# Performance work log

Hardware: AMD Instinct MI355X
Metric: run time of the kernel (lower is better)

Reference implementation:

```python
import jax, jax.numpy as jnp
import numpy as np

T = 32            # num_tsteps
B = 8192          # batch_size
W_IN0, W_OUT0 = 36, 18
W_IN1, W_OUT1 = 18, 8
TILE0, TILE1 = 2, 1
BETA = (0.95, 0.95)
TH = (0.55, 0.25)
Q = 15000.0       # sephia mrr_Q
ER_DB = 20.0      # sephia extinction ratio
IL_DB = 0.0       # sephia insertion loss
SHIFT_PM = -250.0 # sephia resonance shift per unit spike
P_UNITY = 1e-4    # dbm_to_watt(-10): optical power per WDM channel at unit input


def _lif(inp, mem, beta, th):
    # snntorch Leaky, reset_mechanism='zero', reset_delay=True:
    # reset decided from incoming mem, membrane zeroed before leak+integrate.
    reset = (mem > th).astype(inp.dtype)
    mem_new = (beta * mem + inp) * (1.0 - reset)
    spk = (mem_new > th).astype(inp.dtype)
    return spk, mem_new


def _allpass(spk, wl_nm):
    # All-pass MRR modulator: spike shifts the ring resonance by SHIFT_PM.
    # Normalized detuning delta = shift / (FWHM/2), FWHM = lambda / Q.
    fwhm_pm = wl_nm * 1e3 / Q                      # [C]
    delta = (spk * SHIFT_PM) / (0.5 * fwhm_pm)     # [B, C]
    gamma = 10.0 ** (-ER_DB / 20.0)                # on-resonance amplitude (ER)
    il = 10.0 ** (-IL_DB / 20.0)                   # insertion loss factor
    return (il * (1j * delta + gamma) / (1j * delta + 1.0)).astype(jnp.complex64)


def setup_inputs() -> dict:
    key = jax.random.key(0)
    ks = jax.random.split(key, 6)
    return {
        "x_in": jax.random.uniform(ks[0], (T, B, W_IN0), jnp.float32),
        "W0": jax.random.uniform(ks[1], (TILE0, W_IN0 // TILE0, W_OUT0 * 2 // TILE0), jnp.float32),
        "d0": jax.random.normal(ks[2], (TILE0, W_OUT0 // TILE0), jnp.float32) * 5e3,
        "W1": jax.random.uniform(ks[3], (TILE1, W_IN1 // TILE1, W_OUT1 * 2 // TILE1), jnp.float32),
        "d1": jax.random.normal(ks[4], (TILE1, W_OUT1 // TILE1), jnp.float32) * 5e3,
        "peak_powers_dbm": jax.random.uniform(ks[5], (W_IN0,), jnp.float32, -15.0, -5.0),
    }


def reference(x_in, W0, d0, W1, d1, peak_powers_dbm):
    wl0 = 1550.0 + 0.8 * jnp.arange(W_OUT0, dtype=jnp.float32)   # MRR resonance wavelengths (nm)
    # sephia_inputs: sqrt(dbm_to_watt(P_dbm) * 1e6) field amplitude per channel
    amp0 = jnp.sqrt((10.0 ** (peak_powers_dbm[:W_OUT0] / 10.0) / 1000.0) * 1e6)
    S0 = W_OUT0 * 2 // TILE0   # 18 spatial channels after EO broadcast
    S1 = W_OUT1 * 2 // TILE1   # 16 spatial channels into layer 1

    def step(carry, x_t):
        mem0, mem1 = carry
        b = x_t.shape[0]
        # --- EO conversion + layer 0 MRR weight bank (power domain) ---
        p_in = x_t * P_UNITY                                     # [B, 36] optical power
        p0 = jnp.broadcast_to(p_in[:, :, None], (b, W_IN0, S0)).reshape(b, TILE0, W_IN0 // TILE0, S0)
        I0 = jnp.einsum('btws,tws->bts', p0, W0)                 # photocurrents [B,2,18]
        cur0 = ((I0[..., 0::2] - I0[..., 1::2]) * d0).reshape(b, W_OUT0)  # balanced PDs + Diagonal
        spk0, mem0 = _lif(cur0, mem0, BETA[0], TH[0])
        # --- SEPhIA all-pass MRR modulation of comb lines ---
        lo = _allpass(spk0, wl0) * amp0.astype(jnp.complex64)    # [B, 18] complex field
        pw0 = jnp.abs(lo) ** 2                                   # detected power == spike record
        # --- post-SEPhIA broadcast + layer 1 weight bank ---
        p1 = jnp.broadcast_to(pw0[:, :, None], (b, W_IN1, S1)).reshape(b, TILE1, W_IN1 // TILE1, S1)
        I1 = jnp.einsum('btws,tws->bts', p1, W1)                 # [B,1,16]
        cur1 = ((I1[..., 0::2] - I1[..., 1::2]) * d1).reshape(b, W_OUT1)
        spk1, mem1 = _lif(cur1, mem1, BETA[1], TH[1])
        return (mem0, mem1), (pw0, spk1, mem0, mem1)

    mem0 = jnp.zeros((x_in.shape[1], W_OUT0), x_in.dtype)
    mem1 = jnp.zeros((x_in.shape[1], W_OUT1), x_in.dtype)
    _, (spks0, spks1, mems0, mems1) = jax.lax.scan(step, (mem0, mem1), x_in)
    return spks0, spks1, mems0, mems1
```

## Files before the change

kernel.cpp:

```cpp
#include <hip/hip_runtime.h>


namespace {
constexpr int Tn = 32;
constexpr int Bn = 8192;
constexpr int O_PW = 0;
constexpr int O_S1 = Tn * Bn * 18;
constexpr int O_M0 = O_S1 + Tn * Bn * 8;
constexpr int O_M1 = O_M0 + Tn * Bn * 18;
}

__global__ __launch_bounds__(256, 1)
void oesnn_kernel(const float* __restrict__ x_in,
                  const float* __restrict__ W0g,
                  const float* __restrict__ d0g,
                  const float* __restrict__ W1g,
                  const float* __restrict__ d1g,
                  const float* __restrict__ peakg,
                  float* __restrict__ out)
{
    const int lt  = threadIdx.x & 63;
    const int tid = blockIdx.x * 256 + threadIdx.x;
    const int b   = tid >> 3;
    const int sub = tid & 7;
    const int tl  = sub >> 2;
    const int q   = sub & 3;
    const int j0  = (q == 0) ? 0 : (2 * q + 1);
    const int nj  = (q == 0) ? 3 : 2;

    float w0e[3][18], w0o[3][18], dd0[3], pon[3], poff[3];
    #pragma unroll
    for (int j = 0; j < 3; ++j) {
        const int jc = (j < nj) ? (j0 + j) : j0;
        dd0[j] = d0g[tl * 9 + jc];
        #pragma unroll
        for (int w = 0; w < 18; ++w) {
            const float2 p = *(const float2*)(W0g + ((tl * 18 + w) * 18 + 2 * jc));
            w0e[j][w] = p.x;
            w0o[j][w] = p.y;
        }
        const int c = tl * 9 + jc;
        const float wl    = 1550.0f + 0.8f * (float)c;
        const float halfw = 0.5f * (wl * 1e3f / 15000.0f);
        const float amp   = sqrtf((exp10f(peakg[c] / 10.0f) / 1000.0f) * 1e6f);
        {
            const float lr = 0.1f * amp;
            const float a  = sqrtf(lr * lr);
            poff[j] = a * a;
        }
        {
            const float delta = -250.0f / halfw;
            const float den = fmaf(delta, delta, 1.0f);
            const float qr  = fmaf(delta, delta, 0.1f) / den;
            const float qi  = (delta - 0.1f * delta) / den;
            const float lr = qr * amp, li = qi * amp;
            const float a  = sqrtf(fmaf(lr, lr, li * li));
            pon[j] = a * a;
        }
    }

    float w1e[18], w1o[18];
    #pragma unroll
    for (int w = 0; w < 18; ++w) {
        const float2 pp = *(const float2*)(W1g + w * 16 + 2 * sub);
        w1e[w] = pp.x;
        w1o[w] = pp.y;
    }
    const float dd1 = d1g[sub];

    const int basel = lt & ~7;

    float pon_f[18], poff_f[18];
    #pragma unroll
    for (int c = 0; c < 18; ++c) {
        const int tlc = c / 9, jc2 = c % 9;
        const int qo  = (jc2 < 3) ? 0 : ((jc2 - 1) / 2);
        const int st  = (qo == 0) ? 0 : (2 * qo + 1);
        const int r   = jc2 - st;
        pon_f[c]  = __shfl(pon[r],  basel + tlc * 4 + qo, 64);
        poff_f[c] = __shfl(poff[r], basel + tlc * 4 + qo, 64);
    }

    float dd1p = dd1;
    #pragma unroll
    for (int j = 0; j < 3; ++j) {
        #pragma unroll
        for (int w = 0; w < 18; ++w) {
            asm volatile("" : "+v"(w0e[j][w]));
            asm volatile("" : "+v"(w0o[j][w]));
        }
        asm volatile("" : "+v"(dd0[j]));
        asm volatile("" : "+v"(pon[j]));
        asm volatile("" : "+v"(poff[j]));
    }
    #pragma unroll
    for (int w = 0; w < 18; ++w) {
        asm volatile("" : "+v"(w1e[w]));
        asm volatile("" : "+v"(w1o[w]));
        asm volatile("" : "+v"(pon_f[w]));
        asm volatile("" : "+v"(poff_f[w]));
    }
    asm volatile("" : "+v"(dd1p));

    float mem0[3] = {0.f, 0.f, 0.f};
    float mem1 = 0.f;

    const float* xp = x_in + (size_t)b * 36 + tl * 18;
    float* opw = out + O_PW + (size_t)b * 18 + tl * 9 + j0;
    float* om0 = out + O_M0 + (size_t)b * 18 + tl * 9 + j0;
    float* os1 = out + O_S1 + (size_t)b * 8 + sub;
    float* om1 = out + O_M1 + (size_t)b * 8 + sub;

    float2 xv[9];
    #pragma unroll
    for (int k = 0; k < 9; ++k) xv[k] = *(const float2*)(xp + 2 * k);

    #pragma unroll 1
    for (int t = 0; t < Tn; ++t) {
        float p[18];
        #pragma unroll
        for (int k = 0; k < 9; ++k) {
            p[2 * k]     = xv[k].x * 1e-4f;
            p[2 * k + 1] = xv[k].y * 1e-4f;
        }
        xp += Bn * 36;
        if (t < Tn - 1) {
            #pragma unroll
            for (int k = 0; k < 9; ++k) xv[k] = *(const float2*)(xp + 2 * k);
        }

        float pwv[3];
        int   spk[3];
        #pragma unroll
        for (int j = 0; j < 3; ++j) {
            float se = 0.f, so = 0.f;
            #pragma unroll
            for (int w = 0; w < 18; ++w) {
                se = fmaf(p[w], w0e[j][w], se);
                so = fmaf(p[w], w0o[j][w], so);
            }
            const float c0 = (se - so) * dd0[j];
            const float m  = mem0[j];
            const float m2 = (m > 0.55f) ? 0.0f : fmaf(0.95f, m, c0);
            mem0[j] = m2;
            spk[j]  = (m2 > 0.55f) ? 1 : 0;
            pwv[j]  = spk[j] ? pon[j] : poff[j];
        }

        #pragma unroll
        for (int j = 0; j < 3; ++j) {
            if (j < nj) {
                opw[j] = pwv[j];
                om0[j] = mem0[j];
            }
        }

        unsigned long long bm0 = __ballot(spk[0]);
        unsigned long long bm1 = __ballot(spk[1]);
        unsigned long long bm2 = __ballot(spk[2]);
        const unsigned int g0 = (unsigned int)(bm0 >> basel);
        const unsigned int g1 = (unsigned int)(bm1 >> basel);
        const unsigned int g2 = (unsigned int)(bm2 >> basel);

        float i1e = 0.f, i1o = 0.f;
        #pragma unroll
        for (int c = 0; c < 18; ++c) {
            const int tlc = c / 9, jc2 = c % 9;
            const int qo  = (jc2 < 3) ? 0 : ((jc2 - 1) / 2);
            const int st  = (qo == 0) ? 0 : (2 * qo + 1);
            const int r   = jc2 - st;
            const unsigned int gm = (r == 0) ? g0 : ((r == 1) ? g1 : g2);
            const float pwc = ((gm >> (tlc * 4 + qo)) & 1u) ? pon_f[c] : poff_f[c];
            i1e = fmaf(pwc, w1e[c], i1e);
            i1o = fmaf(pwc, w1o[c], i1o);
        }

        const float c1 = (i1e - i1o) * dd1p;
        const float m  = mem1;
        const float m2 = (m > 0.25f) ? 0.0f : fmaf(0.95f, m, c1);
        mem1 = m2;
        *os1 = (m2 > 0.25f) ? 1.0f : 0.0f;
        *om1 = m2;

        opw += Bn * 18;
        om0 += Bn * 18;
        os1 += Bn * 8;
        om1 += Bn * 8;
    }
}

extern "C" void kernel_launch(void* const* d_in, const int* in_sizes, int n_in,
                              void* d_out, int out_size, void* d_ws, size_t ws_size,
                              hipStream_t stream) {
    (void)in_sizes; (void)n_in; (void)out_size; (void)d_ws; (void)ws_size;
    const float* x  = (const float*)d_in[0];
    const float* W0 = (const float*)d_in[1];
    const float* d0 = (const float*)d_in[2];
    const float* W1 = (const float*)d_in[3];
    const float* d1 = (const float*)d_in[4];
    const float* pk = (const float*)d_in[5];
    float* out = (float*)d_out;

    dim3 grid(Bn * 8 / 256), block(256);
    hipLaunchKernelGGL(oesnn_kernel, grid, block, 0, stream,
                       x, W0, d0, W1, d1, pk, out);
}
```

Baseline: 120.5 us.

## Stage x_in loads and pw/mem0 stores through per-wave LDS for coalescing

Each wavefront now stages four timesteps of its 8-batch x_in slab into a double-buffered LDS region with coalesced float4 loads. Per-thread inputs are read from LDS instead of strided global float2 loads. The pw0 and mem0 outputs are buffered in LDS and written back as contiguous float4 rows every four steps. This targets uncoalesced global traffic, at the cost of more LDS use, intra-wave LDS ordering without explicit barriers, and bursty store phases.

```diff
diff --git a/kernel.cpp b/kernel.cpp
--- a/kernel.cpp
+++ b/kernel.cpp
@@ -8,6 +8,9 @@
 constexpr int O_S1 = Tn * Bn * 18;
 constexpr int O_M0 = O_S1 + Tn * Bn * 8;
 constexpr int O_M1 = O_M0 + Tn * Bn * 18;
+constexpr int WSLAB = 3456;
+constexpr int PWOFF = 2304;
+constexpr int M0OFF = 2880;
 }
 
 __global__ __launch_bounds__(256, 1)
@@ -27,6 +30,11 @@
     const int q   = sub & 3;
     const int j0  = (q == 0) ? 0 : (2 * q + 1);
     const int nj  = (q == 0) ? 3 : 2;
+    const int e   = lt >> 3;
+    const int b0  = (tid & ~63) >> 3;
+
+    __shared__ float lds[4 * WSLAB];
+    float* wl = lds + (threadIdx.x >> 6) * WSLAB;
 
     float w0e[3][18], w0o[3][18], dd0[3], pon[3], poff[3];
     #pragma unroll
@@ -40,8 +48,8 @@
             w0o[j][w] = p.y;
         }
         const int c = tl * 9 + jc;
-        const float wl    = 1550.0f + 0.8f * (float)c;
-        const float halfw = 0.5f * (wl * 1e3f / 15000.0f);
+        const float wl_   = 1550.0f + 0.8f * (float)c;
+        const float halfw = 0.5f * (wl_ * 1e3f / 15000.0f);
         const float amp   = sqrtf((exp10f(peakg[c] / 10.0f) / 1000.0f) * 1e6f);
         {
             const float lr = 0.1f * amp;
@@ -105,28 +113,70 @@
     float mem0[3] = {0.f, 0.f, 0.f};
     float mem1 = 0.f;
 
-    const float* xp = x_in + (size_t)b * 36 + tl * 18;
-    float* opw = out + O_PW + (size_t)b * 18 + tl * 9 + j0;
-    float* om0 = out + O_M0 + (size_t)b * 18 + tl * 9 + j0;
     float* os1 = out + O_S1 + (size_t)b * 8 + sub;
     float* om1 = out + O_M1 + (size_t)b * 8 + sub;
 
+    auto stage = [&](int sT) {
+        const int buf = sT & 1;
+        #pragma unroll
+        for (int tt = 0; tt < 4; ++tt) {
+            const float4* gs = (const float4*)(x_in +
+                ((size_t)(4 * sT + tt) * Bn + b0) * 36);
+            float* dst = wl + buf * 1152 + tt * 288;
+            const float4 va = gs[lt];
+            *(float4*)(dst + lt * 4) = va;
+            if (lt < 8) {
+                const float4 vb = gs[64 + lt];
+                *(float4*)(dst + 256 + lt * 4) = vb;
+            }
+        }
+    };
+
+    auto flushf = [&](int sD) {
+        #pragma unroll
+        for (int tt = 0; tt < 4; ++tt) {
+            if (lt < 36) {
+                const float4 v = *(const float4*)(wl + PWOFF + tt * 144 + lt * 4);
+                ((float4*)(out + O_PW +
+                    ((size_t)(4 * sD + tt) * Bn + b0) * 18))[lt] = v;
+                const float4 u = *(const float4*)(wl + M0OFF + tt * 144 + lt * 4);
+                ((float4*)(out + O_M0 +
+                    ((size_t)(4 * sD + tt) * Bn + b0) * 18))[lt] = u;
+            }
+        }
+    };
+
+    stage(0);
+
     float2 xv[9];
-    #pragma unroll
-    for (int k = 0; k < 9; ++k) xv[k] = *(const float2*)(xp + 2 * k);
+    {
+        const float* xb = wl + e * 36 + tl * 18;
+        #pragma unroll
+        for (int k = 0; k < 9; ++k) xv[k] = *(const float2*)(xb + 2 * k);
+    }
 
     #pragma unroll 1
-    for (int t = 0; t < Tn; ++t) {
+    for (int it = 0; it < Tn; ++it) {
+        const int s  = it >> 2;
+        const int tt = it & 3;
+
+        if (tt == 0) {
+            if (s > 0) flushf(s - 1);
+            if (s < 7) stage(s + 1);
+        }
+
         float p[18];
         #pragma unroll
         for (int k = 0; k < 9; ++k) {
             p[2 * k]     = xv[k].x * 1e-4f;
             p[2 * k + 1] = xv[k].y * 1e-4f;
         }
-        xp += Bn * 36;
-        if (t < Tn - 1) {
+        if (it + 1 < Tn) {
+            const int nb  = ((it + 1) >> 2) & 1;
+            const int ntt = (it + 1) & 3;
+            const float* xb = wl + nb * 1152 + ntt * 288 + e * 36 + tl * 18;
             #pragma unroll
-            for (int k = 0; k < 9; ++k) xv[k] = *(const float2*)(xp + 2 * k);
+            for (int k = 0; k < 9; ++k) xv[k] = *(const float2*)(xb + 2 * k);
         }
 
         float pwv[3];
@@ -150,14 +200,15 @@
         #pragma unroll
         for (int j = 0; j < 3; ++j) {
             if (j < nj) {
-                opw[j] = pwv[j];
-                om0[j] = mem0[j];
-            }
-        }
-
-        unsigned long long bm0 = __ballot(spk[0]);
-        unsigned long long bm1 = __ballot(spk[1]);
-        unsigned long long bm2 = __ballot(spk[2]);
+                const int ci = e * 18 + tl * 9 + j0 + j;
+                wl[PWOFF + tt * 144 + ci] = pwv[j];
+                wl[M0OFF + tt * 144 + ci] = mem0[j];
+            }
+        }
+
+        const unsigned long long bm0 = __ballot(spk[0]);
+        const unsigned long long bm1 = __ballot(spk[1]);
+        const unsigned long long bm2 = __ballot(spk[2]);
         const unsigned int g0 = (unsigned int)(bm0 >> basel);
         const unsigned int g1 = (unsigned int)(bm1 >> basel);
         const unsigned int g2 = (unsigned int)(bm2 >> basel);
@@ -181,12 +232,11 @@
         mem1 = m2;
         *os1 = (m2 > 0.25f) ? 1.0f : 0.0f;
         *om1 = m2;
-
-        opw += Bn * 18;
-        om0 += Bn * 18;
         os1 += Bn * 8;
         om1 += Bn * 8;
     }
+
+    flushf(7);
 }
 
 extern "C" void kernel_launch(void* const* d_in, const int* in_sizes, int n_in,
```

Result: slower. 127.2 us (+5.5%).

## Stage all timesteps of x into LDS per 64-thread block up front

Applied to the files above, without the earlier changes.

Blocks shrink to a single 64-lane wavefront covering 8 batch rows, and the grid grows from 256 to 1024 blocks. Each block first copies all 32 timesteps of its x rows into shared memory with coalesced float4 loads, then the time loop reads x from LDS instead of doing strided global float2 loads every step. This is meant to cut global-load latency and uncoalesced traffic inside the sequential time loop. In exchange it adds a serial prologue with 36KB of LDS per block, which can limit how many blocks fit per CU, and there is no barrier after the fill, which is only safe because each block is one wavefront.

```diff
diff --git a/kernel.cpp b/kernel.cpp
--- a/kernel.cpp
+++ b/kernel.cpp
@@ -10,7 +10,7 @@
 constexpr int O_M1 = O_M0 + Tn * Bn * 18;
 }
 
-__global__ __launch_bounds__(256, 1)
+__global__ __launch_bounds__(64, 1)
 void oesnn_kernel(const float* __restrict__ x_in,
                   const float* __restrict__ W0g,
                   const float* __restrict__ d0g,
@@ -19,14 +19,25 @@
                   const float* __restrict__ peakg,
                   float* __restrict__ out)
 {
-    const int lt  = threadIdx.x & 63;
-    const int tid = blockIdx.x * 256 + threadIdx.x;
-    const int b   = tid >> 3;
-    const int sub = tid & 7;
+    const int lt  = threadIdx.x;
+    const int b0  = blockIdx.x * 8;
+    const int b   = b0 + (lt >> 3);
+    const int e   = lt >> 3;
+    const int sub = lt & 7;
     const int tl  = sub >> 2;
     const int q   = sub & 3;
     const int j0  = (q == 0) ? 0 : (2 * q + 1);
     const int nj  = (q == 0) ? 3 : 2;
+
+    __shared__ float xs[Tn * 288];
+
+    #pragma unroll 4
+    for (int t = 0; t < Tn; ++t) {
+        const float4* gs = (const float4*)(x_in + ((size_t)t * Bn + b0) * 36);
+        float4* dst = (float4*)(xs + t * 288);
+        dst[lt] = gs[lt];
+        if (lt < 8) dst[64 + lt] = gs[64 + lt];
+    }
 
     float w0e[3][18], w0o[3][18], dd0[3], pon[3], poff[3];
     #pragma unroll
@@ -105,15 +116,15 @@
     float mem0[3] = {0.f, 0.f, 0.f};
     float mem1 = 0.f;
 
-    const float* xp = x_in + (size_t)b * 36 + tl * 18;
     float* opw = out + O_PW + (size_t)b * 18 + tl * 9 + j0;
     float* om0 = out + O_M0 + (size_t)b * 18 + tl * 9 + j0;
     float* os1 = out + O_S1 + (size_t)b * 8 + sub;
     float* om1 = out + O_M1 + (size_t)b * 8 + sub;
 
+    const float* xb0 = xs + e * 36 + tl * 18;
     float2 xv[9];
     #pragma unroll
-    for (int k = 0; k < 9; ++k) xv[k] = *(const float2*)(xp + 2 * k);
+    for (int k = 0; k < 9; ++k) xv[k] = *(const float2*)(xb0 + 2 * k);
 
     #pragma unroll 1
     for (int t = 0; t < Tn; ++t) {
@@ -123,10 +134,10 @@
             p[2 * k]     = xv[k].x * 1e-4f;
             p[2 * k + 1] = xv[k].y * 1e-4f;
         }
-        xp += Bn * 36;
         if (t < Tn - 1) {
+            const float* xb = xs + (t + 1) * 288 + e * 36 + tl * 18;
             #pragma unroll
-            for (int k = 0; k < 9; ++k) xv[k] = *(const float2*)(xp + 2 * k);
+            for (int k = 0; k < 9; ++k) xv[k] = *(const float2*)(xb + 2 * k);
         }
 
         float pwv[3];
@@ -155,9 +166,9 @@
             }
         }
 
-        unsigned long long bm0 = __ballot(spk[0]);
-        unsigned long long bm1 = __ballot(spk[1]);
-        unsigned long long bm2 = __ballot(spk[2]);
+        const unsigned long long bm0 = __ballot(spk[0]);
+        const unsigned long long bm1 = __ballot(spk[1]);
+        const unsigned long long bm2 = __ballot(spk[2]);
         const unsigned int g0 = (unsigned int)(bm0 >> basel);
         const unsigned int g1 = (unsigned int)(bm1 >> basel);
         const unsigned int g2 = (unsigned int)(bm2 >> basel);
@@ -201,7 +212,7 @@
     const float* pk = (const float*)d_in[5];
     float* out = (float*)d_out;
 
-    dim3 grid(Bn * 8 / 256), block(256);
+    dim3 grid(Bn / 8), block(64);
     hipLaunchKernelGGL(oesnn_kernel, grid, block, 0, stream,
                        x, W0, d0, W1, d1, pk, out);
 }
```

Result: slower. 127.7 us (+6.0%).
